# Kernel optimization log

Measured on AMD Instinct MI355X. Metric: run time of the kernel, lower is better.

The kernel has to match this reference:

```python
import jax, jax.numpy as jnp
import numpy as np

N_QUBITS = 4
DIM = 1 << N_QUBITS  # 16


def _apply1(state, gate, q):
    # state: [B, 16] complex; gate: [2,2] or [B,2,2]; q: qubit index (0 = MSB)
    B = state.shape[0]
    left = 1 << q
    right = 1 << (N_QUBITS - q - 1)
    s = state.reshape(B, left, 2, right)
    if gate.ndim == 2:
        out = jnp.einsum('ij,bajc->baic', gate, s)
    else:
        out = jnp.einsum('bij,bajc->baic', gate, s)
    return out.reshape(B, DIM)


def _cnot(state, c, t):
    # flip target axis where control bit == 1
    B = state.shape[0]
    s = state.reshape((B,) + (2,) * N_QUBITS)
    s0 = jax.lax.index_in_dim(s, 0, c + 1, keepdims=True)
    s1 = jax.lax.index_in_dim(s, 1, c + 1, keepdims=True)
    s1 = jnp.flip(s1, axis=t + 1)
    return jnp.concatenate([s0, s1], axis=c + 1).reshape(B, DIM)


def _ry(theta):
    # theta: [B] -> [B,2,2] complex
    c = jnp.cos(theta / 2)
    s = jnp.sin(theta / 2)
    g = jnp.stack([jnp.stack([c, -s], -1), jnp.stack([s, c], -1)], -2)
    return g.astype(jnp.complex64)


def _rz(theta):
    e0 = jnp.exp(-1j * theta.astype(jnp.complex64) / 2)
    e1 = jnp.exp(1j * theta.astype(jnp.complex64) / 2)
    z = jnp.zeros_like(e0)
    return jnp.stack([jnp.stack([e0, z], -1), jnp.stack([z, e1], -1)], -2)


def _u3(theta, phi, lam):
    # scalar params -> [2,2] complex
    th = theta.astype(jnp.complex64)
    ph = phi.astype(jnp.complex64)
    la = lam.astype(jnp.complex64)
    c = jnp.cos(th / 2)
    s = jnp.sin(th / 2)
    return jnp.array([[1.0, 0.0], [0.0, 0.0]], jnp.complex64) * c \
        + jnp.array([[0.0, -1.0], [0.0, 0.0]], jnp.complex64) * (jnp.exp(1j * la) * s) \
        + jnp.array([[0.0, 0.0], [1.0, 0.0]], jnp.complex64) * (jnp.exp(1j * ph) * s) \
        + jnp.array([[0.0, 0.0], [0.0, 1.0]], jnp.complex64) * (jnp.exp(1j * (ph + la)) * c)


_H = (jnp.array([[1.0, 1.0], [1.0, -1.0]], jnp.float32) / np.sqrt(2.0)).astype(jnp.complex64)


def _circuit(ry_ang, rz_ang, u3_params):
    # ry_ang, rz_ang: [B, 4]; u3_params: [4, 3]
    B = ry_ang.shape[0]
    state = jnp.zeros((B, DIM), jnp.complex64).at[:, 0].set(1.0)
    for q in range(N_QUBITS):
        state = _apply1(state, _H, q)
    for q in range(N_QUBITS):
        state = _apply1(state, _ry(ry_ang[:, q]), q)
    for q in range(N_QUBITS):
        state = _apply1(state, _rz(rz_ang[:, q]), q)
    for q in range(N_QUBITS):  # cnot_ring step=1
        state = _cnot(state, q, (q + 1) % N_QUBITS)
    for q in range(N_QUBITS):  # cnot_ring step=2
        state = _cnot(state, q, (q + 2) % N_QUBITS)
    for q in range(N_QUBITS):
        state = _apply1(state, _u3(u3_params[q, 0], u3_params[q, 1], u3_params[q, 2]), q)
    # Z expectations on each wire
    probs = jnp.abs(state) ** 2  # [B, 16]
    probs = probs.reshape((B,) + (2,) * N_QUBITS)
    exps = []
    for q in range(N_QUBITS):
        axes = tuple(a for a in range(1, N_QUBITS + 1) if a != q + 1)
        p = jnp.sum(probs, axis=axes)  # [B, 2]
        exps.append(p[:, 0] - p[:, 1])
    return jnp.stack(exps, axis=1)  # [B, 4]


def setup_inputs() -> dict:
    key = jax.random.key(0)
    k = jax.random.split(key, 6)
    B = 32768
    input_features = jax.random.normal(k[0], (B, 512), jnp.float32)
    pre_w = jax.random.normal(k[1], (N_QUBITS, 512), jnp.float32) / np.sqrt(512.0)
    pre_b = jnp.zeros((N_QUBITS,), jnp.float32)
    u3_params = jax.random.uniform(k[2], (N_QUBITS, 3), jnp.float32, 0.0, 2.0 * np.pi)
    post_w = jax.random.normal(k[3], (2, N_QUBITS), jnp.float32) / np.sqrt(float(N_QUBITS))
    post_b = jnp.zeros((2,), jnp.float32)
    return {"input_features": input_features, "pre_w": pre_w, "pre_b": pre_b,
            "u3_params": u3_params, "post_w": post_w, "post_b": post_b}


def reference(input_features, pre_w, pre_b, u3_params, post_w, post_b):
    pre_out = input_features @ pre_w.T + pre_b              # [B, 4]
    q_in = jnp.tanh(pre_out / 10.0) * (np.pi / 2.0)          # [B, 4]
    ry_ang = jnp.arctan(q_in)
    rz_ang = jnp.arctan(q_in * q_in)
    q_out = _circuit(ry_ang, rz_ang, u3_params)              # [B, 4] real
    return q_out @ post_w.T + post_b                         # [B, 2]
```

## Files before the change

### kernel.cpp

```cpp
#include <hip/hip_runtime.h>
#include <math.h>

#define NQ 4
#define DIM 16
#define K 512

__global__ __launch_bounds__(256) void qnet_gemm(const float* __restrict__ x,
                                                 const float* __restrict__ w,
                                                 const float* __restrict__ bias,
                                                 float* __restrict__ pre_out,
                                                 int B) {
    const int wid  = (int)((blockIdx.x * blockDim.x + threadIdx.x) >> 6);
    const int lane = (int)(threadIdx.x & 63);
    const int row0 = wid * 4;
    if (row0 >= B) return;

    float4 wf[NQ][2];
#pragma unroll
    for (int q = 0; q < NQ; ++q) {
#pragma unroll
        for (int h = 0; h < 2; ++h)
            wf[q][h] = *(const float4*)(w + q * K + h * 256 + lane * 4);
    }

    float acc[4][NQ];
#pragma unroll
    for (int r = 0; r < 4; ++r) {
        int row = row0 + r;
        if (row >= B) row = B - 1;
        const float* xr = x + (size_t)row * K;
        float4 x0 = *(const float4*)(xr + lane * 4);
        float4 x1 = *(const float4*)(xr + 256 + lane * 4);
#pragma unroll
        for (int q = 0; q < NQ; ++q) {
            acc[r][q] = x0.x * wf[q][0].x + x0.y * wf[q][0].y
                      + x0.z * wf[q][0].z + x0.w * wf[q][0].w
                      + x1.x * wf[q][1].x + x1.y * wf[q][1].y
                      + x1.z * wf[q][1].z + x1.w * wf[q][1].w;
        }
    }

    const int l1 = lane & 1;
    const int l2 = lane & 2;
    float v[4];
#pragma unroll
    for (int r = 0; r < 4; ++r) {
        float a01k = l1 ? acc[r][1] : acc[r][0];
        float a01s = l1 ? acc[r][0] : acc[r][1];
        a01k += __shfl_xor(a01s, 1, 64);
        float a23k = l1 ? acc[r][3] : acc[r][2];
        float a23s = l1 ? acc[r][2] : acc[r][3];
        a23k += __shfl_xor(a23s, 1, 64);
        float vk = l2 ? a23k : a01k;
        float vs = l2 ? a01k : a23k;
        vk += __shfl_xor(vs, 2, 64);
#pragma unroll
        for (int off = 4; off <= 32; off <<= 1)
            vk += __shfl_xor(vk, off, 64);
        v[r] = vk;
    }

    if (lane < 16) {
        const int r = lane >> 2;
        const int q = lane & 3;
        float vr = (r == 0) ? v[0] : (r == 1) ? v[1] : (r == 2) ? v[2] : v[3];
        const int row = row0 + r;
        if (row < B) pre_out[(size_t)row * 4 + q] = vr + bias[q];
    }
}

__global__ __launch_bounds__(256) void qnet_circuit(const float* __restrict__ pre_out,
                                                    const float* __restrict__ u3p,
                                                    const float* __restrict__ post_w,
                                                    const float* __restrict__ post_b,
                                                    float* __restrict__ out,
                                                    int B) {
    int b = (int)(blockIdx.x * blockDim.x + threadIdx.x);
    if (b >= B) return;

    float4 p4 = *(const float4*)(pre_out + (size_t)b * 4);
    float pre[NQ] = {p4.x, p4.y, p4.z, p4.w};

    float ry[NQ], rz[NQ];
#pragma unroll
    for (int q = 0; q < NQ; ++q) {
        float z = pre[q] * 0.1f;
        float t = 1.0f - 2.0f / (__expf(2.0f * z) + 1.0f);
        float qi = t * 1.5707963267948966f;
        ry[q] = atanf(qi);
        rz[q] = atanf(qi * qi);
    }

    float sr[DIM], si[DIM];
#pragma unroll
    for (int i = 0; i < DIM; ++i) { sr[i] = 0.25f; si[i] = 0.0f; }

#pragma unroll
    for (int q = 0; q < NQ; ++q) {
        float c, s;
        __sincosf(ry[q] * 0.5f, &s, &c);
        const int m = 1 << (3 - q);
#pragma unroll
        for (int i = 0; i < DIM; ++i) {
            if (i & m) continue;
            const int j = i | m;
            float r0 = sr[i], i0 = si[i], r1 = sr[j], i1 = si[j];
            sr[i] = c * r0 - s * r1;  si[i] = c * i0 - s * i1;
            sr[j] = s * r0 + c * r1;  si[j] = s * i0 + c * i1;
        }
    }

#pragma unroll
    for (int q = 0; q < NQ; ++q) {
        float c, s;
        __sincosf(rz[q] * 0.5f, &s, &c);
        const int m = 1 << (3 - q);
#pragma unroll
        for (int i = 0; i < DIM; ++i) {
            const float sg = (i & m) ? s : -s;
            float r = sr[i], im = si[i];
            sr[i] = c * r - sg * im;
            si[i] = c * im + sg * r;
        }
    }

    const int cn_c[8] = {0, 1, 2, 3, 0, 1, 2, 3};
    const int cn_t[8] = {1, 2, 3, 0, 2, 3, 0, 1};
#pragma unroll
    for (int k = 0; k < 8; ++k) {
        const int cm = 1 << (3 - cn_c[k]);
        const int tm = 1 << (3 - cn_t[k]);
#pragma unroll
        for (int i = 0; i < DIM; ++i) {
            if ((i & cm) && !(i & tm)) {
                const int j = i | tm;
                float tr = sr[i]; sr[i] = sr[j]; sr[j] = tr;
                float ti = si[i]; si[i] = si[j]; si[j] = ti;
            }
        }
    }

#pragma unroll
    for (int q = 0; q < NQ; ++q) {
        float th = u3p[q * 3 + 0], ph = u3p[q * 3 + 1], la = u3p[q * 3 + 2];
        float ct, st, cl, sl, cp, sp, cpl, spl;
        __sincosf(th * 0.5f, &st, &ct);
        __sincosf(la, &sl, &cl);
        __sincosf(ph, &sp, &cp);
        __sincosf(ph + la, &spl, &cpl);
        const float g01r = -cl * st, g01i = -sl * st;
        const float g10r = cp * st,  g10i = sp * st;
        const float g11r = cpl * ct, g11i = spl * ct;
        const int m = 1 << (3 - q);
#pragma unroll
        for (int i = 0; i < DIM; ++i) {
            if (i & m) continue;
            const int j = i | m;
            float r0 = sr[i], i0 = si[i], r1 = sr[j], i1 = si[j];
            sr[i] = ct * r0 + g01r * r1 - g01i * i1;
            si[i] = ct * i0 + g01r * i1 + g01i * r1;
            sr[j] = g10r * r0 - g10i * i0 + g11r * r1 - g11i * i1;
            si[j] = g10r * i0 + g10i * r0 + g11r * i1 + g11i * r1;
        }
    }

    float ex[NQ] = {0.f, 0.f, 0.f, 0.f};
#pragma unroll
    for (int i = 0; i < DIM; ++i) {
        const float p2 = sr[i] * sr[i] + si[i] * si[i];
#pragma unroll
        for (int q = 0; q < NQ; ++q)
            ex[q] += (i & (1 << (3 - q))) ? -p2 : p2;
    }

    float o0 = post_b[0], o1 = post_b[1];
#pragma unroll
    for (int q = 0; q < NQ; ++q) {
        o0 += ex[q] * post_w[q];
        o1 += ex[q] * post_w[4 + q];
    }
    *(float2*)(out + (size_t)b * 2) = make_float2(o0, o1);
}

extern "C" void kernel_launch(void* const* d_in, const int* in_sizes, int n_in,
                              void* d_out, int out_size, void* d_ws, size_t ws_size,
                              hipStream_t stream) {
    const float* x      = (const float*)d_in[0];
    const float* pre_w  = (const float*)d_in[1];
    const float* pre_b  = (const float*)d_in[2];
    const float* u3p    = (const float*)d_in[3];
    const float* post_w = (const float*)d_in[4];
    const float* post_b = (const float*)d_in[5];
    float* out = (float*)d_out;

    const int B = in_sizes[0] / K;
    float* pre_out = (float*)d_ws;

    {
        int rows_per_block = 16;
        int blocks = (B + rows_per_block - 1) / rows_per_block;
        qnet_gemm<<<blocks, 256, 0, stream>>>(x, pre_w, pre_b, pre_out, B);
    }
    {
        int threads = 256;
        int blocks = (B + threads - 1) / threads;
        qnet_circuit<<<blocks, threads, 0, stream>>>(pre_out, u3p, post_w, post_b, out, B);
    }
}
```

Baseline: 103.4 us.

## Fuse GEMM projection and circuit simulation into one kernel via LDS

Merges the two kernels into a single launch: each 256-thread block computes 16 rows of the projection into shared memory, then 16 threads of that block run the circuit simulation for those rows. This removes the second kernel launch and the global round-trip of the intermediate pre_out buffer. In exchange only 16 of 256 threads do the circuit work per block, and waves in that block stall on a barrier, so the heavy per-row circuit arithmetic runs at low occupancy and may serialize after the memory phase.

After: 102.3 us. About the same (-1.1%).

```diff
diff --git a/kernel.cpp b/kernel.cpp
--- a/kernel.cpp
+++ b/kernel.cpp
@@ -5,88 +5,90 @@
 #define DIM 16
 #define K 512
 
-__global__ __launch_bounds__(256) void qnet_gemm(const float* __restrict__ x,
-                                                 const float* __restrict__ w,
-                                                 const float* __restrict__ bias,
-                                                 float* __restrict__ pre_out,
-                                                 int B) {
-    const int wid  = (int)((blockIdx.x * blockDim.x + threadIdx.x) >> 6);
+__global__ __launch_bounds__(256) void qnet_fused(const float* __restrict__ x,
+                                                  const float* __restrict__ w,
+                                                  const float* __restrict__ bias,
+                                                  const float* __restrict__ u3p,
+                                                  const float* __restrict__ post_w,
+                                                  const float* __restrict__ post_b,
+                                                  float* __restrict__ out,
+                                                  int B) {
+    __shared__ float lds_pre[64];
+
+    const int wave = (int)(threadIdx.x >> 6);
     const int lane = (int)(threadIdx.x & 63);
-    const int row0 = wid * 4;
-    if (row0 >= B) return;
-
-    float4 wf[NQ][2];
-#pragma unroll
-    for (int q = 0; q < NQ; ++q) {
-#pragma unroll
-        for (int h = 0; h < 2; ++h)
-            wf[q][h] = *(const float4*)(w + q * K + h * 256 + lane * 4);
-    }
-
-    float acc[4][NQ];
-#pragma unroll
-    for (int r = 0; r < 4; ++r) {
-        int row = row0 + r;
-        if (row >= B) row = B - 1;
-        const float* xr = x + (size_t)row * K;
-        float4 x0 = *(const float4*)(xr + lane * 4);
-        float4 x1 = *(const float4*)(xr + 256 + lane * 4);
+    const int block_row0 = (int)blockIdx.x * 16;
+    const int row0 = block_row0 + wave * 4;
+
+    if (row0 < B) {
+        float4 wf[NQ][2];
 #pragma unroll
         for (int q = 0; q < NQ; ++q) {
-            acc[r][q] = x0.x * wf[q][0].x + x0.y * wf[q][0].y
-                      + x0.z * wf[q][0].z + x0.w * wf[q][0].w
-                      + x1.x * wf[q][1].x + x1.y * wf[q][1].y
-                      + x1.z * wf[q][1].z + x1.w * wf[q][1].w;
-        }
-    }
-
-    const int l1 = lane & 1;
-    const int l2 = lane & 2;
-    float v[4];
-#pragma unroll
-    for (int r = 0; r < 4; ++r) {
-        float a01k = l1 ? acc[r][1] : acc[r][0];
-        float a01s = l1 ? acc[r][0] : acc[r][1];
-        a01k += __shfl_xor(a01s, 1, 64);
-        float a23k = l1 ? acc[r][3] : acc[r][2];
-        float a23s = l1 ? acc[r][2] : acc[r][3];
-        a23k += __shfl_xor(a23s, 1, 64);
-        float vk = l2 ? a23k : a01k;
-        float vs = l2 ? a01k : a23k;
-        vk += __shfl_xor(vs, 2, 64);
-#pragma unroll
-        for (int off = 4; off <= 32; off <<= 1)
-            vk += __shfl_xor(vk, off, 64);
-        v[r] = vk;
-    }
-
-    if (lane < 16) {
-        const int r = lane >> 2;
-        const int q = lane & 3;
-        float vr = (r == 0) ? v[0] : (r == 1) ? v[1] : (r == 2) ? v[2] : v[3];
-        const int row = row0 + r;
-        if (row < B) pre_out[(size_t)row * 4 + q] = vr + bias[q];
-    }
-}
-
-__global__ __launch_bounds__(256) void qnet_circuit(const float* __restrict__ pre_out,
-                                                    const float* __restrict__ u3p,
-                                                    const float* __restrict__ post_w,
-                                                    const float* __restrict__ post_b,
-                                                    float* __restrict__ out,
-                                                    int B) {
-    int b = (int)(blockIdx.x * blockDim.x + threadIdx.x);
+#pragma unroll
+            for (int h = 0; h < 2; ++h)
+                wf[q][h] = *(const float4*)(w + q * K + h * 256 + lane * 4);
+        }
+
+        float acc[4][NQ];
+#pragma unroll
+        for (int r = 0; r < 4; ++r) {
+            int row = row0 + r;
+            if (row >= B) row = B - 1;
+            const float* xr = x + (size_t)row * K;
+            float4 x0 = *(const float4*)(xr + lane * 4);
+            float4 x1 = *(const float4*)(xr + 256 + lane * 4);
+#pragma unroll
+            for (int q = 0; q < NQ; ++q) {
+                acc[r][q] = x0.x * wf[q][0].x + x0.y * wf[q][0].y
+                          + x0.z * wf[q][0].z + x0.w * wf[q][0].w
+                          + x1.x * wf[q][1].x + x1.y * wf[q][1].y
+                          + x1.z * wf[q][1].z + x1.w * wf[q][1].w;
+            }
+        }
+
+        const int l1 = lane & 1;
+        const int l2 = lane & 2;
+        float v[4];
+#pragma unroll
+        for (int r = 0; r < 4; ++r) {
+            float a01k = l1 ? acc[r][1] : acc[r][0];
+            float a01s = l1 ? acc[r][0] : acc[r][1];
+            a01k += __shfl_xor(a01s, 1, 64);
+            float a23k = l1 ? acc[r][3] : acc[r][2];
+            float a23s = l1 ? acc[r][2] : acc[r][3];
+            a23k += __shfl_xor(a23s, 1, 64);
+            float vk = l2 ? a23k : a01k;
+            float vs = l2 ? a01k : a23k;
+            vk += __shfl_xor(vs, 2, 64);
+#pragma unroll
+            for (int off = 4; off <= 32; off <<= 1)
+                vk += __shfl_xor(vk, off, 64);
+            v[r] = vk;
+        }
+
+        if (lane < 16) {
+            const int r = lane >> 2;
+            const int q = lane & 3;
+            float vr = (r == 0) ? v[0] : (r == 1) ? v[1] : (r == 2) ? v[2] : v[3];
+            lds_pre[wave * 16 + lane] = vr + bias[q];
+        }
+    }
+    __syncthreads();
+
+    const int t = (int)threadIdx.x;
+    if (t >= 16) return;
+    const int b = block_row0 + t;
     if (b >= B) return;
 
-    float4 p4 = *(const float4*)(pre_out + (size_t)b * 4);
-    float pre[NQ] = {p4.x, p4.y, p4.z, p4.w};
+    float pre[NQ] = {lds_pre[t * 4 + 0], lds_pre[t * 4 + 1],
+                     lds_pre[t * 4 + 2], lds_pre[t * 4 + 3]};
 
     float ry[NQ], rz[NQ];
 #pragma unroll
     for (int q = 0; q < NQ; ++q) {
         float z = pre[q] * 0.1f;
-        float t = 1.0f - 2.0f / (__expf(2.0f * z) + 1.0f);
-        float qi = t * 1.5707963267948966f;
+        float tnh = 1.0f - 2.0f / (__expf(2.0f * z) + 1.0f);
+        float qi = tnh * 1.5707963267948966f;
         ry[q] = atanf(qi);
         rz[q] = atanf(qi * qi);
     }
@@ -194,16 +196,8 @@
     float* out = (float*)d_out;
 
     const int B = in_sizes[0] / K;
-    float* pre_out = (float*)d_ws;
-
-    {
-        int rows_per_block = 16;
-        int blocks = (B + rows_per_block - 1) / rows_per_block;
-        qnet_gemm<<<blocks, 256, 0, stream>>>(x, pre_w, pre_b, pre_out, B);
-    }
-    {
-        int threads = 256;
-        int blocks = (B + threads - 1) / threads;
-        qnet_circuit<<<blocks, threads, 0, stream>>>(pre_out, u3p, post_w, post_b, out, B);
-    }
+
+    const int rows_per_block = 16;
+    const int blocks = (B + rows_per_block - 1) / rows_per_block;
+    qnet_fused<<<blocks, 256, 0, stream>>>(x, pre_w, pre_b, u3p, post_w, post_b, out, B);
 }
```
